# Optimization experiments

Measured on AMD Instinct MI355X. Metric: run time of the kernel, lower is better.

The kernel has to match this reference:

```python
import jax, jax.numpy as jnp
import numpy as np

LATENT = 96  # num_features // reduce_ratio
RDK = LATENT ** 0.5


def setup_inputs() -> dict:
    key = jax.random.key(0)
    k1, k2, k3, k4, k5 = jax.random.split(key, 5)
    B, C, H, W = 8, 192, 64, 64
    x = jax.random.normal(k1, (B, C, H, W), dtype=jnp.float32)
    # transform: Conv2d(C, 3*latent, kernel=1) -> weight [3*latent, C]
    Wt = jax.random.normal(k2, (3 * LATENT, C), dtype=jnp.float32) * 0.05
    bt = jax.random.normal(k3, (3 * LATENT,), dtype=jnp.float32) * 0.05
    # decode: Conv2d(latent, C, kernel=1) -> weight [C, latent]
    Wd = jax.random.normal(k4, (C, LATENT), dtype=jnp.float32) * 0.05
    bd = jax.random.normal(k5, (C,), dtype=jnp.float32) * 0.05
    return {"x": x, "Wt": Wt, "bt": bt, "Wd": Wd, "bd": bd}


def reference(x, Wt, bt, Wd, bd):
    B, C, H, W = x.shape
    N = H * W
    # 1x1 conv QKV projection: [B, 3*latent, H, W]
    t = jnp.einsum('bchw,oc->bohw', x, Wt) + bt[None, :, None, None]
    Q = t[:, :LATENT]                      # [B, latent, H, W]
    V = t[:, LATENT:2 * LATENT]            # [B, latent, H, W]
    K = t[:, 2 * LATENT:]                  # [B, latent, H, W]
    Qf = Q.reshape(B, LATENT, N)
    Vf = V.reshape(B, LATENT, N)
    Kf = K.reshape(B, LATENT, N)
    # score[b, q, k] = sum_c Q[b,c,q] * K[b,c,k]
    score = jnp.einsum('bcq,bck->bqk', Qf, Kf) / jnp.asarray(RDK, x.dtype)
    # softmax over the QUERY axis (dim=1), as in the original code
    index = jax.nn.softmax(score, axis=1)  # [B, Nq, Nk]
    # output[b, c, k] = sum_q V[b,c,q] * index[b,q,k]
    out = jnp.einsum('bcq,bqk->bck', Vf, index).reshape(B, LATENT, H, W)
    # decode 1x1 conv + residual
    out = jnp.einsum('bchw,oc->bohw', out, Wd) + bd[None, :, None, None]
    return out + x
```

## Files before the change

### kernel.cpp

```cpp
#include <hip/hip_runtime.h>

#define LATENT 96
#define NCH    192
#define O3     288
#define NSEQ   4096
#define NB     8

typedef short bf16_t;
typedef __attribute__((ext_vector_type(8))) short  short8;
typedef __attribute__((ext_vector_type(4))) short  short4_t;
typedef __attribute__((ext_vector_type(4))) float  f32x4;

#define C2SCALE 0.14724447f

__device__ __forceinline__ short f2bf(float f) {
  union { float f; unsigned u; } v; v.f = f;
  unsigned r = v.u + 0x7FFFu + ((v.u >> 16) & 1u);
  return (short)(r >> 16);
}

__device__ __forceinline__ unsigned pk2bf(float lo, float hi) {
  unsigned r;
  asm("v_cvt_pk_bf16_f32 %0, %1, %2" : "=v"(r) : "v"(lo), "v"(hi));
  return r;
}

__device__ __forceinline__ f32x4 mfma16(short8 a, short8 b, f32x4 c) {
  return __builtin_amdgcn_mfma_f32_16x16x32_bf16(a, b, c, 0, 0, 0);
}

__global__ __launch_bounds__(256) void k1_qkv(const float* __restrict__ x,
                                              const float* __restrict__ Wt,
                                              const float* __restrict__ bt,
                                              bf16_t* __restrict__ tT,
                                              bf16_t* __restrict__ tV) {
  const int tid = threadIdx.x;
  const int li = tid & 15, lg = (tid >> 4) & 3, wid = tid >> 6;
  const int b = blockIdx.y, n0 = blockIdx.x * 64;

  __shared__ __align__(16) char sm1[51200];
  bf16_t* Xs = (bf16_t*)sm1;
  bf16_t* Ws = (bf16_t*)(sm1 + 25600);
  bf16_t* Tts = Ws;
  bf16_t* Tvs = Ws + 64 * 72;

  const float* xb = x + (size_t)b * NCH * NSEQ + n0;
  for (int e = tid; e < NCH * 16; e += 256) {
    int c = e >> 4, nq = e & 15;
    float4 xv = *(const float4*)(xb + (size_t)c * NSEQ + nq * 4);
    Xs[(4 * nq + 0) * 200 + c] = f2bf(xv.x);
    Xs[(4 * nq + 1) * 200 + c] = f2bf(xv.y);
    Xs[(4 * nq + 2) * 200 + c] = f2bf(xv.z);
    Xs[(4 * nq + 3) * 200 + c] = f2bf(xv.w);
  }

  bf16_t* tTb = tT + (size_t)b * NSEQ * O3;
  bf16_t* tVb = tV + (size_t)b * LATENT * NSEQ;

  for (int mi = 0; mi < 5; ++mi) {
    const int m0 = mi * 64;
    __syncthreads();
    for (int e = tid; e < 64 * 48; e += 256) {
      int r = e / 48, cq = e % 48;
      int o = m0 + r;
      float4 wv = make_float4(0.f, 0.f, 0.f, 0.f);
      if (o < O3) wv = *(const float4*)(Wt + (size_t)o * NCH + 4 * cq);
      Ws[r * 200 + 4 * cq + 0] = f2bf(wv.x);
      Ws[r * 200 + 4 * cq + 1] = f2bf(wv.y);
      Ws[r * 200 + 4 * cq + 2] = f2bf(wv.z);
      Ws[r * 200 + 4 * cq + 3] = f2bf(wv.w);
    }
    __syncthreads();

    f32x4 acc[4];
    #pragma unroll
    for (int s = 0; s < 4; ++s) { acc[s][0]=0.f; acc[s][1]=0.f; acc[s][2]=0.f; acc[s][3]=0.f; }
    __builtin_amdgcn_s_setprio(1);
    #pragma unroll
    for (int kk = 0; kk < 6; ++kk) {
      short8 ax = *(const short8*)(Xs + (16 * wid + li) * 200 + 32 * kk + 8 * lg);
      #pragma unroll
      for (int sub = 0; sub < 4; ++sub) {
        short8 bw = *(const short8*)(Ws + (16 * sub + li) * 200 + 32 * kk + 8 * lg);
        acc[sub] = mfma16(ax, bw, acc[sub]);
      }
    }
    __builtin_amdgcn_s_setprio(0);
    __syncthreads();

    #pragma unroll
    for (int sub = 0; sub < 4; ++sub) {
      int orel = 16 * sub + li;
      int o = m0 + orel;
      float bo = (o < O3) ? bt[o] : 0.f;
      #pragma unroll
      for (int r = 0; r < 4; ++r) {
        int nn = 16 * wid + 4 * lg + r;
        float v = acc[sub][r] + bo;
        bf16_t bv = f2bf(o >= 2 * LATENT ? v * C2SCALE : v);
        Tts[nn * 72 + orel] = bv;
        if (o >= LATENT && o < 2 * LATENT) Tvs[orel * 72 + nn] = bv;
      }
    }
    __syncthreads();

    const int W = (m0 + 64 <= O3) ? 64 : (O3 - m0);
    const int CPR = W / 8;
    for (int ch = tid; ch < 64 * CPR; ch += 256) {
      int row = ch / CPR, cc = ch % CPR;
      *(short8*)(tTb + (size_t)(n0 + row) * O3 + m0 + cc * 8) =
          *(const short8*)(Tts + row * 72 + cc * 8);
    }
    if (mi == 1 || mi == 2) {
      const int orelbase = (mi == 1) ? 32 : 0;
      const int vbase    = (mi == 1) ? 0  : 32;
      const int R        = (mi == 1) ? 32 : 64;
      for (int ch = tid; ch < R * 8; ch += 256) {
        int r = ch / 8, cc = ch % 8;
        *(short8*)(tVb + (size_t)(vbase + r) * NSEQ + n0 + cc * 8) =
            *(const short8*)(Tvs + (orelbase + r) * 72 + cc * 8);
      }
    }
  }
}

__global__ __launch_bounds__(512, 1) void k2_attn(const bf16_t* __restrict__ tT,
                                                  const bf16_t* __restrict__ tV,
                                                  bf16_t* __restrict__ aoT) {
  __shared__ __align__(16) char smem[54272];
  bf16_t* Qs0 = (bf16_t*)smem;
  bf16_t* Qs1 = (bf16_t*)(smem + 13312);
  bf16_t* Vs0 = (bf16_t*)(smem + 26624);
  bf16_t* Vs1 = (bf16_t*)(smem + 40448);

  const int tid = threadIdx.x;
  const int lane = tid & 63, li = lane & 15, lg = lane >> 4;
  const int wid = tid >> 6, g = wid >> 2, w4 = wid & 3;
  const int gt = tid & 255;

  const int myid = blockIdx.x + 32 * blockIdx.y;
  const int b = myid & 7;
  const int i0 = (myid >> 3) * 128;

  const bf16_t* tTb = tT + (size_t)b * NSEQ * O3;
  const bf16_t* tVb = tV + (size_t)b * LATENT * NSEQ;

  short8 kb[2][3];
  #pragma unroll
  for (int ib = 0; ib < 2; ++ib)
    #pragma unroll
    for (int kk = 0; kk < 3; ++kk)
      kb[ib][kk] = *(const short8*)(tTb +
          (size_t)(i0 + 32 * w4 + 16 * ib + li) * O3 + 2 * LATENT + 32 * kk + 8 * lg);

  bf16_t* Qg = g ? Qs1 : Qs0;
  bf16_t* Vg = g ? Vs1 : Vs0;

  int qlds[3], qglb[3], vlds[6], vglb[6];
  #pragma unroll
  for (int h = 0; h < 3; ++h) {
    int id = gt + 256 * h, row = id / 12, cc = id % 12;
    qlds[h] = row * 104 + cc * 8;
    qglb[h] = row * O3 + cc * 8;
  }
  #pragma unroll
  for (int h = 0; h < 6; ++h) {
    int id = gt + 256 * h, c = id >> 4, q4 = (id & 15) * 4;
    int lg2 = (q4 >> 2) & 3, hh = (q4 >> 4) & 1, ks = q4 >> 5;
    vlds[h] = c * 72 + ks * 32 + lg2 * 8 + hh * 4;
    vglb[h] = c * NSEQ + q4;
  }

  short8 qr[3];
  short4_t vr[6];
  {
    const int q0 = g * 64;
    #pragma unroll
    for (int h = 0; h < 3; ++h)
      qr[h] = *(const short8*)(tTb + (size_t)q0 * O3 + qglb[h]);
    #pragma unroll
    for (int h = 0; h < 6; ++h)
      vr[h] = *(const short4_t*)(tVb + q0 + vglb[h]);
  }

  f32x4 Oa[2][6];
  #pragma unroll
  for (int ib = 0; ib < 2; ++ib)
    #pragma unroll
    for (int s = 0; s < 6; ++s) { Oa[ib][s][0]=0.f; Oa[ib][s][1]=0.f; Oa[ib][s][2]=0.f; Oa[ib][s][3]=0.f; }
  float m2[2] = {-3.0e38f, -3.0e38f};
  float l[2] = {0.f, 0.f};

  for (int t = 0; t < 32; ++t) {
    __syncthreads();
    #pragma unroll
    for (int h = 0; h < 3; ++h) *(short8*)(Qg + qlds[h]) = qr[h];
    #pragma unroll
    for (int h = 0; h < 6; ++h) *(short4_t*)(Vg + vlds[h]) = vr[h];
    __syncthreads();

    if (t < 31) {
      const int q0n = (2 * (t + 1) + g) * 64;
      #pragma unroll
      for (int h = 0; h < 3; ++h)
        qr[h] = *(const short8*)(tTb + (size_t)q0n * O3 + qglb[h]);
      #pragma unroll
      for (int h = 0; h < 6; ++h)
        vr[h] = *(const short4_t*)(tVb + q0n + vglb[h]);
    }

    f32x4 S[2][4];
    #pragma unroll
    for (int ib = 0; ib < 2; ++ib)
      #pragma unroll
      for (int s = 0; s < 4; ++s) { S[ib][s][0]=0.f; S[ib][s][1]=0.f; S[ib][s][2]=0.f; S[ib][s][3]=0.f; }
    __builtin_amdgcn_s_setprio(1);
    #pragma unroll
    for (int kk = 0; kk < 3; ++kk) {
      short8 aq[4];
      #pragma unroll
      for (int s = 0; s < 4; ++s)
        aq[s] = *(const short8*)(Qg + (16 * s + li) * 104 + 32 * kk + 8 * lg);
      #pragma unroll
      for (int ib = 0; ib < 2; ++ib)
        #pragma unroll
        for (int s = 0; s < 4; ++s)
          S[ib][s] = mfma16(aq[s], kb[ib][kk], S[ib][s]);
    }
    __builtin_amdgcn_s_setprio(0);

    float p[2][16];
    #pragma unroll
    for (int ib = 0; ib < 2; ++ib) {
      float tm = S[ib][0][0];
      #pragma unroll
      for (int s = 0; s < 4; ++s)
        #pragma unroll
        for (int r = 0; r < 4; ++r) {
          p[ib][4 * s + r] = S[ib][s][r];
          tm = fmaxf(tm, S[ib][s][r]);
        }
      tm = fmaxf(tm, __shfl_xor(tm, 16));
      tm = fmaxf(tm, __shfl_xor(tm, 32));
      float mnew = fmaxf(m2[ib], tm);
      float scl = __builtin_amdgcn_exp2f(m2[ib] - mnew);
      float ls = 0.f;
      #pragma unroll
      for (int k = 0; k < 16; ++k) {
        p[ib][k] = __builtin_amdgcn_exp2f(p[ib][k] - mnew);
        ls += p[ib][k];
      }
      ls += __shfl_xor(ls, 16);
      ls += __shfl_xor(ls, 32);
      l[ib] = l[ib] * scl + ls;
      m2[ib] = mnew;
      #pragma unroll
      for (int s = 0; s < 6; ++s) {
        Oa[ib][s][0] *= scl; Oa[ib][s][1] *= scl; Oa[ib][s][2] *= scl; Oa[ib][s][3] *= scl;
      }
    }

    __builtin_amdgcn_s_setprio(1);
    #pragma unroll
    for (int ks = 0; ks < 2; ++ks) {
      union { unsigned u[4]; short8 s8; } bp0, bp1;
      #pragma unroll
      for (int j = 0; j < 4; ++j) {
        bp0.u[j] = pk2bf(p[0][8 * ks + 2 * j], p[0][8 * ks + 2 * j + 1]);
        bp1.u[j] = pk2bf(p[1][8 * ks + 2 * j], p[1][8 * ks + 2 * j + 1]);
      }
      #pragma unroll
      for (int sub = 0; sub < 6; ++sub) {
        short8 av = *(const short8*)(Vg + (16 * sub + li) * 72 + ks * 32 + lg * 8);
        Oa[0][sub] = mfma16(av, bp0.s8, Oa[0][sub]);
        Oa[1][sub] = mfma16(av, bp1.s8, Oa[1][sub]);
      }
    }
    __builtin_amdgcn_s_setprio(0);
  }

  float* Op = (float*)smem;
  float* Ms = (float*)(smem + 49152);
  float* Ls = Ms + 128;
  __syncthreads();
  if (g == 1) {
    #pragma unroll
    for (int ib = 0; ib < 2; ++ib) {
      float* dst = Op + (size_t)((w4 * 64 + lane) * 2 + ib) * 24;
      #pragma unroll
      for (int sub = 0; sub < 6; ++sub) *(f32x4*)(dst + 4 * sub) = Oa[ib][sub];
      if (lg == 0) {
        int ir = 32 * w4 + 16 * ib + li;
        Ms[ir] = m2[ib]; Ls[ir] = l[ib];
      }
    }
  }
  __syncthreads();
  if (g == 0) {
    #pragma unroll
    for (int ib = 0; ib < 2; ++ib) {
      int ir = 32 * w4 + 16 * ib + li;
      float m1 = Ms[ir], l1 = Ls[ir];
      const float* src = Op + (size_t)((w4 * 64 + lane) * 2 + ib) * 24;
      float mM = fmaxf(m2[ib], m1);
      float s0 = __builtin_amdgcn_exp2f(m2[ib] - mM);
      float s1 = __builtin_amdgcn_exp2f(m1 - mM);
      float linv = 1.f / (l[ib] * s0 + l1 * s1);
      #pragma unroll
      for (int sub = 0; sub < 6; ++sub)
        #pragma unroll
        for (int r = 0; r < 4; ++r)
          Oa[ib][sub][r] = (Oa[ib][sub][r] * s0 + src[4 * sub + r] * s1) * linv;
    }
  }
  __syncthreads();
  bf16_t* AoS = (bf16_t*)smem;
  if (g == 0) {
    #pragma unroll
    for (int ib = 0; ib < 2; ++ib) {
      int ir = 32 * w4 + 16 * ib + li;
      #pragma unroll
      for (int sub = 0; sub < 6; ++sub)
        #pragma unroll
        for (int r = 0; r < 4; ++r)
          AoS[ir * 104 + 16 * sub + 4 * lg + r] = f2bf(Oa[ib][sub][r]);
    }
  }
  __syncthreads();
  bf16_t* aoTb = aoT + (size_t)b * NSEQ * LATENT;
  for (int ch = tid; ch < 1536; ch += 512) {
    int row = ch / 12, cc = ch % 12;
    *(short8*)(aoTb + (size_t)(i0 + row) * LATENT + cc * 8) =
        *(const short8*)(AoS + row * 104 + cc * 8);
  }
}

__global__ __launch_bounds__(256) void k3_proj(const bf16_t* __restrict__ aoT,
                                               const float* __restrict__ Wd,
                                               const float* __restrict__ bd,
                                               const float* __restrict__ x,
                                               float* __restrict__ out) {
  const int tid = threadIdx.x;
  const int li = tid & 15, lg = (tid >> 4) & 3, wid = tid >> 6;
  const int b = blockIdx.z, m0 = blockIdx.y * 64, n0 = blockIdx.x * 64;

  __shared__ __align__(16) char sm3[26624];
  bf16_t* Ws = (bf16_t*)sm3;
  bf16_t* As = (bf16_t*)(sm3 + 13312);
  float*  Os = (float*)sm3;

  const bf16_t* aob = aoT + (size_t)b * NSEQ * LATENT;
  for (int ch = tid; ch < 768; ch += 256) {
    int row = ch / 12, cc = ch % 12;
    *(short8*)(As + row * 104 + cc * 8) =
        *(const short8*)(aob + (size_t)(n0 + row) * LATENT + cc * 8);
  }
  for (int e = tid; e < 64 * 24; e += 256) {
    int r = e / 24, cq = e % 24;
    float4 wv = *(const float4*)(Wd + (size_t)(m0 + r) * LATENT + 4 * cq);
    Ws[r * 104 + 4 * cq + 0] = f2bf(wv.x);
    Ws[r * 104 + 4 * cq + 1] = f2bf(wv.y);
    Ws[r * 104 + 4 * cq + 2] = f2bf(wv.z);
    Ws[r * 104 + 4 * cq + 3] = f2bf(wv.w);
  }
  __syncthreads();

  f32x4 acc[4];
  #pragma unroll
  for (int s = 0; s < 4; ++s) { acc[s][0]=0.f; acc[s][1]=0.f; acc[s][2]=0.f; acc[s][3]=0.f; }
  __builtin_amdgcn_s_setprio(1);
  #pragma unroll
  for (int kk = 0; kk < 3; ++kk) {
    short8 aw = *(const short8*)(Ws + (16 * wid + li) * 104 + 32 * kk + 8 * lg);
    #pragma unroll
    for (int sub = 0; sub < 4; ++sub) {
      short8 ba = *(const short8*)(As + (16 * sub + li) * 104 + 32 * kk + 8 * lg);
      acc[sub] = mfma16(aw, ba, acc[sub]);
    }
  }
  __builtin_amdgcn_s_setprio(0);
  __syncthreads();

  #pragma unroll
  for (int sub = 0; sub < 4; ++sub)
    #pragma unroll
    for (int r = 0; r < 4; ++r) {
      int o = 16 * wid + 4 * lg + r;
      Os[o * 68 + 16 * sub + li] = acc[sub][r] + bd[m0 + o];
    }
  __syncthreads();

  const float* xb = x + ((size_t)b * NCH + m0) * NSEQ + n0;
  float* ob = out + ((size_t)b * NCH + m0) * NSEQ + n0;
  for (int ch = tid; ch < 64 * 16; ch += 256) {
    int row = ch >> 4, cq = ch & 15;
    float4 xv = *(const float4*)(xb + (size_t)row * NSEQ + 4 * cq);
    const float* os = Os + row * 68 + 4 * cq;
    float4 r4;
    r4.x = os[0] + xv.x;
    r4.y = os[1] + xv.y;
    r4.z = os[2] + xv.z;
    r4.w = os[3] + xv.w;
    *(float4*)(ob + (size_t)row * NSEQ + 4 * cq) = r4;
  }
}

extern "C" void kernel_launch(void* const* d_in, const int* in_sizes, int n_in,
                              void* d_out, int out_size, void* d_ws, size_t ws_size,
                              hipStream_t stream) {
  const float* x  = (const float*)d_in[0];
  const float* Wt = (const float*)d_in[1];
  const float* bt = (const float*)d_in[2];
  const float* Wd = (const float*)d_in[3];
  const float* bd = (const float*)d_in[4];
  float* out = (float*)d_out;

  char* ws = (char*)d_ws;
  const size_t tT_bytes = (size_t)NB * NSEQ * O3 * 2;
  const size_t tV_bytes = (size_t)NB * LATENT * NSEQ * 2;
  bf16_t* tT  = (bf16_t*)ws;
  bf16_t* tV  = (bf16_t*)(ws + tT_bytes);
  bf16_t* aoT = (bf16_t*)(ws + tT_bytes + tV_bytes);

  k1_qkv<<<dim3(64, NB), dim3(256), 0, stream>>>(x, Wt, bt, tT, tV);
  k2_attn<<<dim3(32, NB), dim3(512), 0, stream>>>(tT, tV, aoT);
  k3_proj<<<dim3(64, 3, NB), dim3(256), 0, stream>>>(aoT, Wd, bd, x, out);
}
```

Before: 193.7 us.

## Fuse decode projection into attention kernel and widen attention blocks to 16 waves

The decode 1x1 conv and residual add are folded into the attention kernel, so the intermediate attention output no longer round-trips through global memory and one launch disappears. The attention block grows from 512 to 1024 threads with four query groups, each covering a quarter of the key sequence, merged by a two-level online-softmax reduction. The QKV projection kernel now splits its five output-row tiles across grid blocks, which raises parallelism but makes each block reload and re-convert the x tile. Risks include higher register and LDS pressure at 1024 threads per block and extra reduction synchronisation.

Result: slower. 377.0 us (+94.6%).

```diff
diff --git a/kernel.cpp b/kernel.cpp
--- a/kernel.cpp
+++ b/kernel.cpp
@@ -36,7 +36,8 @@
                                               bf16_t* __restrict__ tV) {
   const int tid = threadIdx.x;
   const int li = tid & 15, lg = (tid >> 4) & 3, wid = tid >> 6;
-  const int b = blockIdx.y, n0 = blockIdx.x * 64;
+  const int b = blockIdx.z, mi = blockIdx.y, n0 = blockIdx.x * 64;
+  const int m0 = mi * 64;
 
   __shared__ __align__(16) char sm1[51200];
   bf16_t* Xs = (bf16_t*)sm1;
@@ -53,97 +54,93 @@
     Xs[(4 * nq + 2) * 200 + c] = f2bf(xv.z);
     Xs[(4 * nq + 3) * 200 + c] = f2bf(xv.w);
   }
+  for (int e = tid; e < 64 * 48; e += 256) {
+    int r = e / 48, cq = e % 48;
+    int o = m0 + r;
+    float4 wv = make_float4(0.f, 0.f, 0.f, 0.f);
+    if (o < O3) wv = *(const float4*)(Wt + (size_t)o * NCH + 4 * cq);
+    Ws[r * 200 + 4 * cq + 0] = f2bf(wv.x);
+    Ws[r * 200 + 4 * cq + 1] = f2bf(wv.y);
+    Ws[r * 200 + 4 * cq + 2] = f2bf(wv.z);
+    Ws[r * 200 + 4 * cq + 3] = f2bf(wv.w);
+  }
+  __syncthreads();
+
+  f32x4 acc[4];
+  #pragma unroll
+  for (int s = 0; s < 4; ++s) { acc[s][0]=0.f; acc[s][1]=0.f; acc[s][2]=0.f; acc[s][3]=0.f; }
+  __builtin_amdgcn_s_setprio(1);
+  #pragma unroll
+  for (int kk = 0; kk < 6; ++kk) {
+    short8 ax = *(const short8*)(Xs + (16 * wid + li) * 200 + 32 * kk + 8 * lg);
+    #pragma unroll
+    for (int sub = 0; sub < 4; ++sub) {
+      short8 bw = *(const short8*)(Ws + (16 * sub + li) * 200 + 32 * kk + 8 * lg);
+      acc[sub] = mfma16(ax, bw, acc[sub]);
+    }
+  }
+  __builtin_amdgcn_s_setprio(0);
+  __syncthreads();
+
+  #pragma unroll
+  for (int sub = 0; sub < 4; ++sub) {
+    int orel = 16 * sub + li;
+    int o = m0 + orel;
+    float bo = (o < O3) ? bt[o] : 0.f;
+    #pragma unroll
+    for (int r = 0; r < 4; ++r) {
+      int nn = 16 * wid + 4 * lg + r;
+      float v = acc[sub][r] + bo;
+      bf16_t bv = f2bf(o >= 2 * LATENT ? v * C2SCALE : v);
+      Tts[nn * 72 + orel] = bv;
+      if (o >= LATENT && o < 2 * LATENT) Tvs[orel * 72 + nn] = bv;
+    }
+  }
+  __syncthreads();
 
   bf16_t* tTb = tT + (size_t)b * NSEQ * O3;
   bf16_t* tVb = tV + (size_t)b * LATENT * NSEQ;
-
-  for (int mi = 0; mi < 5; ++mi) {
-    const int m0 = mi * 64;
-    __syncthreads();
-    for (int e = tid; e < 64 * 48; e += 256) {
-      int r = e / 48, cq = e % 48;
-      int o = m0 + r;
-      float4 wv = make_float4(0.f, 0.f, 0.f, 0.f);
-      if (o < O3) wv = *(const float4*)(Wt + (size_t)o * NCH + 4 * cq);
-      Ws[r * 200 + 4 * cq + 0] = f2bf(wv.x);
-      Ws[r * 200 + 4 * cq + 1] = f2bf(wv.y);
-      Ws[r * 200 + 4 * cq + 2] = f2bf(wv.z);
-      Ws[r * 200 + 4 * cq + 3] = f2bf(wv.w);
-    }
-    __syncthreads();
-
-    f32x4 acc[4];
-    #pragma unroll
-    for (int s = 0; s < 4; ++s) { acc[s][0]=0.f; acc[s][1]=0.f; acc[s][2]=0.f; acc[s][3]=0.f; }
-    __builtin_amdgcn_s_setprio(1);
-    #pragma unroll
-    for (int kk = 0; kk < 6; ++kk) {
-      short8 ax = *(const short8*)(Xs + (16 * wid + li) * 200 + 32 * kk + 8 * lg);
-      #pragma unroll
-      for (int sub = 0; sub < 4; ++sub) {
-        short8 bw = *(const short8*)(Ws + (16 * sub + li) * 200 + 32 * kk + 8 * lg);
-        acc[sub] = mfma16(ax, bw, acc[sub]);
-      }
-    }
-    __builtin_amdgcn_s_setprio(0);
-    __syncthreads();
-
-    #pragma unroll
-    for (int sub = 0; sub < 4; ++sub) {
-      int orel = 16 * sub + li;
-      int o = m0 + orel;
-      float bo = (o < O3) ? bt[o] : 0.f;
-      #pragma unroll
-      for (int r = 0; r < 4; ++r) {
-        int nn = 16 * wid + 4 * lg + r;
-        float v = acc[sub][r] + bo;
-        bf16_t bv = f2bf(o >= 2 * LATENT ? v * C2SCALE : v);
-        Tts[nn * 72 + orel] = bv;
-        if (o >= LATENT && o < 2 * LATENT) Tvs[orel * 72 + nn] = bv;
-      }
-    }
-    __syncthreads();
-
-    const int W = (m0 + 64 <= O3) ? 64 : (O3 - m0);
-    const int CPR = W / 8;
-    for (int ch = tid; ch < 64 * CPR; ch += 256) {
-      int row = ch / CPR, cc = ch % CPR;
-      *(short8*)(tTb + (size_t)(n0 + row) * O3 + m0 + cc * 8) =
-          *(const short8*)(Tts + row * 72 + cc * 8);
-    }
-    if (mi == 1 || mi == 2) {
-      const int orelbase = (mi == 1) ? 32 : 0;
-      const int vbase    = (mi == 1) ? 0  : 32;
-      const int R        = (mi == 1) ? 32 : 64;
-      for (int ch = tid; ch < R * 8; ch += 256) {
-        int r = ch / 8, cc = ch % 8;
-        *(short8*)(tVb + (size_t)(vbase + r) * NSEQ + n0 + cc * 8) =
-            *(const short8*)(Tvs + (orelbase + r) * 72 + cc * 8);
-      }
-    }
-  }
-}
-
-__global__ __launch_bounds__(512, 1) void k2_attn(const bf16_t* __restrict__ tT,
-                                                  const bf16_t* __restrict__ tV,
-                                                  bf16_t* __restrict__ aoT) {
-  __shared__ __align__(16) char smem[54272];
-  bf16_t* Qs0 = (bf16_t*)smem;
-  bf16_t* Qs1 = (bf16_t*)(smem + 13312);
-  bf16_t* Vs0 = (bf16_t*)(smem + 26624);
-  bf16_t* Vs1 = (bf16_t*)(smem + 40448);
-
+  const int W = (m0 + 64 <= O3) ? 64 : (O3 - m0);
+  const int CPR = W / 8;
+  for (int ch = tid; ch < 64 * CPR; ch += 256) {
+    int row = ch / CPR, cc = ch % CPR;
+    *(short8*)(tTb + (size_t)(n0 + row) * O3 + m0 + cc * 8) =
+        *(const short8*)(Tts + row * 72 + cc * 8);
+  }
+  if (mi == 1 || mi == 2) {
+    const int orelbase = (mi == 1) ? 32 : 0;
+    const int vbase    = (mi == 1) ? 0  : 32;
+    const int R        = (mi == 1) ? 32 : 64;
+    for (int ch = tid; ch < R * 8; ch += 256) {
+      int r = ch / 8, cc = ch % 8;
+      *(short8*)(tVb + (size_t)(vbase + r) * NSEQ + n0 + cc * 8) =
+          *(const short8*)(Tvs + (orelbase + r) * 72 + cc * 8);
+    }
+  }
+}
+
+__global__ __launch_bounds__(1024, 4) void k2_attn(const bf16_t* __restrict__ tT,
+                                                   const bf16_t* __restrict__ tV,
+                                                   const float* __restrict__ Wd,
+                                                   const float* __restrict__ bd,
+                                                   const float* __restrict__ x,
+                                                   float* __restrict__ out) {
+  __shared__ __align__(16) char smem[108544];
   const int tid = threadIdx.x;
   const int lane = tid & 63, li = lane & 15, lg = lane >> 4;
-  const int wid = tid >> 6, g = wid >> 2, w4 = wid & 3;
+  const int wid = tid >> 6;
+  const int g = wid >> 2, w4 = wid & 3;
   const int gt = tid & 255;
 
-  const int myid = blockIdx.x + 32 * blockIdx.y;
+  const int myid = blockIdx.x;
   const int b = myid & 7;
   const int i0 = (myid >> 3) * 128;
 
   const bf16_t* tTb = tT + (size_t)b * NSEQ * O3;
   const bf16_t* tVb = tV + (size_t)b * LATENT * NSEQ;
+
+  bf16_t* Qg = (bf16_t*)(smem + g * 13312);
+  bf16_t* Vg = (bf16_t*)(smem + 53248 + g * 13824);
 
   short8 kb[2][3];
   #pragma unroll
@@ -152,9 +149,6 @@
     for (int kk = 0; kk < 3; ++kk)
       kb[ib][kk] = *(const short8*)(tTb +
           (size_t)(i0 + 32 * w4 + 16 * ib + li) * O3 + 2 * LATENT + 32 * kk + 8 * lg);
-
-  bf16_t* Qg = g ? Qs1 : Qs0;
-  bf16_t* Vg = g ? Vs1 : Vs0;
 
   int qlds[3], qglb[3], vlds[6], vglb[6];
   #pragma unroll
@@ -191,7 +185,7 @@
   float m2[2] = {-3.0e38f, -3.0e38f};
   float l[2] = {0.f, 0.f};
 
-  for (int t = 0; t < 32; ++t) {
+  for (int t = 0; t < 16; ++t) {
     __syncthreads();
     #pragma unroll
     for (int h = 0; h < 3; ++h) *(short8*)(Qg + qlds[h]) = qr[h];
@@ -199,8 +193,8 @@
     for (int h = 0; h < 6; ++h) *(short4_t*)(Vg + vlds[h]) = vr[h];
     __syncthreads();
 
-    if (t < 31) {
-      const int q0n = (2 * (t + 1) + g) * 64;
+    if (t < 15) {
+      const int q0n = (4 * (t + 1) + g) * 64;
       #pragma unroll
       for (int h = 0; h < 3; ++h)
         qr[h] = *(const short8*)(tTb + (size_t)q0n * O3 + qglb[h]);
@@ -279,38 +273,86 @@
     __builtin_amdgcn_s_setprio(0);
   }
 
-  float* Op = (float*)smem;
-  float* Ms = (float*)(smem + 49152);
-  float* Ls = Ms + 128;
-  __syncthreads();
-  if (g == 1) {
-    #pragma unroll
-    for (int ib = 0; ib < 2; ++ib) {
-      float* dst = Op + (size_t)((w4 * 64 + lane) * 2 + ib) * 24;
+  float* buf0 = (float*)smem;
+  float* buf1 = (float*)(smem + 53248);
+  float* MsA  = (float*)(smem + 102400);
+
+  __syncthreads();
+  if (g == 1 || g == 3) {
+    float* bufd = (g == 1) ? buf0 : buf1;
+    float* Msd  = MsA + ((g == 1) ? 0 : 256);
+    #pragma unroll
+    for (int ib = 0; ib < 2; ++ib) {
+      float* dst = bufd + ((w4 * 64 + lane) * 2 + ib) * 24;
       #pragma unroll
       for (int sub = 0; sub < 6; ++sub) *(f32x4*)(dst + 4 * sub) = Oa[ib][sub];
       if (lg == 0) {
         int ir = 32 * w4 + 16 * ib + li;
-        Ms[ir] = m2[ib]; Ls[ir] = l[ib];
-      }
-    }
-  }
-  __syncthreads();
+        Msd[ir] = m2[ib]; Msd[128 + ir] = l[ib];
+      }
+    }
+  }
+  __syncthreads();
+  if (g == 0 || g == 2) {
+    const float* bufs = (g == 0) ? buf0 : buf1;
+    const float* Mss  = MsA + ((g == 0) ? 0 : 256);
+    #pragma unroll
+    for (int ib = 0; ib < 2; ++ib) {
+      int ir = 32 * w4 + 16 * ib + li;
+      float m1 = Mss[ir], l1 = Mss[128 + ir];
+      const float* src = bufs + ((w4 * 64 + lane) * 2 + ib) * 24;
+      float mM = fmaxf(m2[ib], m1);
+      float s0 = __builtin_amdgcn_exp2f(m2[ib] - mM);
+      float s1 = __builtin_amdgcn_exp2f(m1 - mM);
+      l[ib] = l[ib] * s0 + l1 * s1;
+      m2[ib] = mM;
+      #pragma unroll
+      for (int sub = 0; sub < 6; ++sub)
+        #pragma unroll
+        for (int r = 0; r < 4; ++r)
+          Oa[ib][sub][r] = Oa[ib][sub][r] * s0 + src[4 * sub + r] * s1;
+    }
+  }
+  __syncthreads();
+  if (g == 2) {
+    #pragma unroll
+    for (int ib = 0; ib < 2; ++ib) {
+      float* dst = buf0 + ((w4 * 64 + lane) * 2 + ib) * 24;
+      #pragma unroll
+      for (int sub = 0; sub < 6; ++sub) *(f32x4*)(dst + 4 * sub) = Oa[ib][sub];
+      if (lg == 0) {
+        int ir = 32 * w4 + 16 * ib + li;
+        MsA[512 + ir] = m2[ib]; MsA[640 + ir] = l[ib];
+      }
+    }
+  }
+  __syncthreads();
+  bf16_t* WdS = (bf16_t*)(smem + 53248);
   if (g == 0) {
     #pragma unroll
     for (int ib = 0; ib < 2; ++ib) {
       int ir = 32 * w4 + 16 * ib + li;
-      float m1 = Ms[ir], l1 = Ls[ir];
-      const float* src = Op + (size_t)((w4 * 64 + lane) * 2 + ib) * 24;
+      float m1 = MsA[512 + ir], l1 = MsA[640 + ir];
+      const float* src = buf0 + ((w4 * 64 + lane) * 2 + ib) * 24;
       float mM = fmaxf(m2[ib], m1);
       float s0 = __builtin_amdgcn_exp2f(m2[ib] - mM);
       float s1 = __builtin_amdgcn_exp2f(m1 - mM);
       float linv = 1.f / (l[ib] * s0 + l1 * s1);
+      s0 *= linv; s1 *= linv;
       #pragma unroll
       for (int sub = 0; sub < 6; ++sub)
         #pragma unroll
         for (int r = 0; r < 4; ++r)
-          Oa[ib][sub][r] = (Oa[ib][sub][r] * s0 + src[4 * sub + r] * s1) * linv;
+          Oa[ib][sub][r] = Oa[ib][sub][r] * s0 + src[4 * sub + r] * s1;
+    }
+  } else {
+    for (int e = tid - 256; e < 192 * 24; e += 768) {
+      int r = e / 24, cq = e % 24;
+      float4 wv = *(const float4*)(Wd + (size_t)r * LATENT + 4 * cq);
+      WdS[r * 104 + 4 * cq + 0] = f2bf(wv.x);
+      WdS[r * 104 + 4 * cq + 1] = f2bf(wv.y);
+      WdS[r * 104 + 4 * cq + 2] = f2bf(wv.z);
+      WdS[r * 104 + 4 * cq + 3] = f2bf(wv.w);
     }
   }
   __syncthreads();
@@ -327,75 +369,41 @@
     }
   }
   __syncthreads();
-  bf16_t* aoTb = aoT + (size_t)b * NSEQ * LATENT;
-  for (int ch = tid; ch < 1536; ch += 512) {
-    int row = ch / 12, cc = ch % 12;
-    *(short8*)(aoTb + (size_t)(i0 + row) * LATENT + cc * 8) =
-        *(const short8*)(AoS + row * 104 + cc * 8);
-  }
-}
-
-__global__ __launch_bounds__(256) void k3_proj(const bf16_t* __restrict__ aoT,
-                                               const float* __restrict__ Wd,
-                                               const float* __restrict__ bd,
-                                               const float* __restrict__ x,
-                                               float* __restrict__ out) {
-  const int tid = threadIdx.x;
-  const int li = tid & 15, lg = (tid >> 4) & 3, wid = tid >> 6;
-  const int b = blockIdx.z, m0 = blockIdx.y * 64, n0 = blockIdx.x * 64;
-
-  __shared__ __align__(16) char sm3[26624];
-  bf16_t* Ws = (bf16_t*)sm3;
-  bf16_t* As = (bf16_t*)(sm3 + 13312);
-  float*  Os = (float*)sm3;
-
-  const bf16_t* aob = aoT + (size_t)b * NSEQ * LATENT;
-  for (int ch = tid; ch < 768; ch += 256) {
-    int row = ch / 12, cc = ch % 12;
-    *(short8*)(As + row * 104 + cc * 8) =
-        *(const short8*)(aob + (size_t)(n0 + row) * LATENT + cc * 8);
-  }
-  for (int e = tid; e < 64 * 24; e += 256) {
-    int r = e / 24, cq = e % 24;
-    float4 wv = *(const float4*)(Wd + (size_t)(m0 + r) * LATENT + 4 * cq);
-    Ws[r * 104 + 4 * cq + 0] = f2bf(wv.x);
-    Ws[r * 104 + 4 * cq + 1] = f2bf(wv.y);
-    Ws[r * 104 + 4 * cq + 2] = f2bf(wv.z);
-    Ws[r * 104 + 4 * cq + 3] = f2bf(wv.w);
-  }
-  __syncthreads();
-
-  f32x4 acc[4];
-  #pragma unroll
-  for (int s = 0; s < 4; ++s) { acc[s][0]=0.f; acc[s][1]=0.f; acc[s][2]=0.f; acc[s][3]=0.f; }
+
+  const int oh = wid >> 3, nb = wid & 7;
+  f32x4 pacc[6];
+  #pragma unroll
+  for (int s = 0; s < 6; ++s) { pacc[s][0]=0.f; pacc[s][1]=0.f; pacc[s][2]=0.f; pacc[s][3]=0.f; }
   __builtin_amdgcn_s_setprio(1);
   #pragma unroll
   for (int kk = 0; kk < 3; ++kk) {
-    short8 aw = *(const short8*)(Ws + (16 * wid + li) * 104 + 32 * kk + 8 * lg);
-    #pragma unroll
-    for (int sub = 0; sub < 4; ++sub) {
-      short8 ba = *(const short8*)(As + (16 * sub + li) * 104 + 32 * kk + 8 * lg);
-      acc[sub] = mfma16(aw, ba, acc[sub]);
+    short8 pa = *(const short8*)(AoS + (16 * nb + li) * 104 + 32 * kk + 8 * lg);
+    #pragma unroll
+    for (int sub = 0; sub < 6; ++sub) {
+      short8 pb = *(const short8*)(WdS + (96 * oh + 16 * sub + li) * 104 + 32 * kk + 8 * lg);
+      pacc[sub] = mfma16(pa, pb, pacc[sub]);
     }
   }
   __builtin_amdgcn_s_setprio(0);
   __syncthreads();
 
-  #pragma unroll
-  for (int sub = 0; sub < 4; ++sub)
-    #pragma unroll
-    for (int r = 0; r < 4; ++r) {
-      int o = 16 * wid + 4 * lg + r;
-      Os[o * 68 + 16 * sub + li] = acc[sub][r] + bd[m0 + o];
-    }
-  __syncthreads();
-
-  const float* xb = x + ((size_t)b * NCH + m0) * NSEQ + n0;
-  float* ob = out + ((size_t)b * NCH + m0) * NSEQ + n0;
-  for (int ch = tid; ch < 64 * 16; ch += 256) {
-    int row = ch >> 4, cq = ch & 15;
+  float* Os = (float*)smem;
+  #pragma unroll
+  for (int sub = 0; sub < 6; ++sub) {
+    int o = 96 * oh + 16 * sub + li;
+    float bo = bd[o];
+    #pragma unroll
+    for (int r = 0; r < 4; ++r)
+      Os[o * 132 + 16 * nb + 4 * lg + r] = pacc[sub][r] + bo;
+  }
+  __syncthreads();
+
+  const float* xb = x + (size_t)b * NCH * NSEQ + i0;
+  float* ob = out + (size_t)b * NCH * NSEQ + i0;
+  for (int ch = tid; ch < 192 * 32; ch += 1024) {
+    int row = ch >> 5, cq = ch & 31;
     float4 xv = *(const float4*)(xb + (size_t)row * NSEQ + 4 * cq);
-    const float* os = Os + row * 68 + 4 * cq;
+    const float* os = Os + row * 132 + 4 * cq;
     float4 r4;
     r4.x = os[0] + xv.x;
     r4.y = os[1] + xv.y;
@@ -417,12 +425,9 @@
 
   char* ws = (char*)d_ws;
   const size_t tT_bytes = (size_t)NB * NSEQ * O3 * 2;
-  const size_t tV_bytes = (size_t)NB * LATENT * NSEQ * 2;
-  bf16_t* tT  = (bf16_t*)ws;
-  bf16_t* tV  = (bf16_t*)(ws + tT_bytes);
-  bf16_t* aoT = (bf16_t*)(ws + tT_bytes + tV_bytes);
-
-  k1_qkv<<<dim3(64, NB), dim3(256), 0, stream>>>(x, Wt, bt, tT, tV);
-  k2_attn<<<dim3(32, NB), dim3(512), 0, stream>>>(tT, tV, aoT);
-  k3_proj<<<dim3(64, 3, NB), dim3(256), 0, stream>>>(aoT, Wd, bd, x, out);
-}
+  bf16_t* tT = (bf16_t*)ws;
+  bf16_t* tV = (bf16_t*)(ws + tT_bytes);
+
+  k1_qkv<<<dim3(64, 5, NB), dim3(256), 0, stream>>>(x, Wt, bt, tT, tV);
+  k2_attn<<<dim3(256), dim3(1024), 0, stream>>>(tT, tV, Wd, bd, x, out);
+}
```
